# Kernel tuning notes

Hardware: AMD Instinct MI355X
Metric: run time of the kernel (lower is better)

Reference implementation:

```python
import jax, jax.numpy as jnp
import numpy as np

BITS = 4        # int4_fullrange
NPACK = 8       # 32-bit container / 4-bit values
BLOCK = 64      # quantization group size (blocksize)
MASK = (1 << BITS) - 1


def _unpack(packed):
    """Unpack int32 words into NPACK 4-bit unsigned values along the last dim.
    packed: (..., P) int32 -> (..., P*NPACK) int32 in [0, 15]."""
    shifts = jnp.arange(NPACK, dtype=jnp.int32) * BITS  # (8,)
    vals = (packed[..., None] >> shifts) & MASK          # (..., P, 8)
    return vals.reshape(*packed.shape[:-1], packed.shape[-1] * NPACK)


def setup_inputs() -> dict:
    key = jax.random.key(0)
    k1, k2, k3, k4, k5 = jax.random.split(key, 5)
    tokens, in_f, out_f = 4096, 4096, 11008
    groups = in_f // BLOCK                      # 64
    x = jax.random.normal(k1, (tokens, in_f), jnp.float32)
    qweight = jax.random.randint(k2, (out_f, in_f // NPACK), 0, 2147483647, jnp.int32)
    qzeros = jax.random.randint(k3, (out_f, groups // NPACK), 0, 2147483647, jnp.int32)
    scales = jax.random.uniform(k4, (out_f, groups), jnp.float32, 0.001, 0.01)
    bias = jax.random.normal(k5, (out_f,), jnp.float32)
    return {"x": x, "qweight": qweight, "qzeros": qzeros, "scales": scales, "bias": bias}


def reference(x, qweight, qzeros, scales, bias):
    # Recover fp32 weight: w[o, g*BLOCK + b] = scales[o, g] * (w_int - zp[o, g])
    out_f, groups = scales.shape
    w_int = _unpack(qweight).astype(jnp.float32)           # (out, in)
    zp = _unpack(qzeros).astype(jnp.float32)               # (out, groups)
    w = (w_int.reshape(out_f, groups, BLOCK) - zp[:, :, None]) * scales[:, :, None]
    w = w.reshape(out_f, groups * BLOCK)                   # (out, in)
    # F.linear(x, w, bias)
    return x @ w.T + bias
```

## Files before the change

### kernel.cpp

```cpp
#include <hip/hip_runtime.h>
#include <stdint.h>

#define M_TOK 4096
#define K_IN  4096
#define N_OUT 11008
#define GROUPS 64
#define WPR 512

#define BM 256
#define BN 256
#define BK 64
#define TM (M_TOK / BM)
#define TN (N_OUT / BN)
#define NWG (TM * TN)
#define KTILES (K_IN / BK)

typedef __bf16 bf16x8 __attribute__((ext_vector_type(8)));
typedef float  f32x4  __attribute__((ext_vector_type(4)));

__device__ __forceinline__ uint16_t f2bf(float f) {
  uint32_t u = __float_as_uint(f);
  u += 0x7FFFu + ((u >> 16) & 1u);
  return (uint16_t)(u >> 16);
}

#define XBLK ((M_TOK * K_IN) / (256 * 8))
#define WBLK ((N_OUT * WPR) / 256)

__global__ __launch_bounds__(256) void prep(const float* __restrict__ x,
                                            const uint32_t* __restrict__ qw,
                                            const uint32_t* __restrict__ qz,
                                            const float* __restrict__ sc,
                                            uint16_t* __restrict__ xb,
                                            uint16_t* __restrict__ wb) {
  if (blockIdx.x < XBLK) {
    size_t i = ((size_t)blockIdx.x * 256 + threadIdx.x) * 8;
    const float4* p = (const float4*)(x + i);
    float4 a = p[0];
    float4 b = p[1];
    uint4 v;
    v.x = (uint32_t)f2bf(a.x) | ((uint32_t)f2bf(a.y) << 16);
    v.y = (uint32_t)f2bf(a.z) | ((uint32_t)f2bf(a.w) << 16);
    v.z = (uint32_t)f2bf(b.x) | ((uint32_t)f2bf(b.y) << 16);
    v.w = (uint32_t)f2bf(b.z) | ((uint32_t)f2bf(b.w) << 16);
    *(uint4*)(xb + i) = v;
  } else {
    int idx = (blockIdx.x - XBLK) * 256 + threadIdx.x;
    int o = idx >> 9;
    int p = idx & 511;
    int g = p >> 3;
    uint32_t zw = qz[o * (GROUPS / 8) + (g >> 3)];
    float zp = (float)((zw >> ((g & 7) * 4)) & 15u);
    float s = sc[o * GROUPS + g];
    float c = -s * zp;
    uint32_t w = qw[idx];
    uint4 v;
    uint32_t r[4];
#pragma unroll
    for (int j = 0; j < 4; j++) {
      float f0 = (float)((w >> (8 * j)) & 15u);
      float f1 = (float)((w >> (8 * j + 4)) & 15u);
      r[j] = (uint32_t)f2bf(fmaf(f0, s, c)) | ((uint32_t)f2bf(fmaf(f1, s, c)) << 16);
    }
    v.x = r[0]; v.y = r[1]; v.z = r[2]; v.w = r[3];
    *(uint4*)(wb + (size_t)idx * 8) = v;
  }
}

#define SBAR()   __builtin_amdgcn_s_barrier()
#define SCHED0() __builtin_amdgcn_sched_barrier(0)
#define WAITV(n) asm volatile("s_waitcnt vmcnt(" #n ")" ::: "memory")
#define WAITL0() asm volatile("s_waitcnt lgkmcnt(0)" ::: "memory")

#define STAGE_A(buf, half, kt) do {                                            \
  _Pragma("unroll")                                                            \
  for (int c_ = 0; c_ < 2; c_++) {                                             \
    const int r_ = (half) * 128 + c_ * 64 + wave * 8;                          \
    __builtin_amdgcn_global_load_lds(                                          \
        (const __attribute__((address_space(1))) uint32_t*)(                   \
            gA + (size_t)r_ * K_IN + (size_t)(kt) * BK),                       \
        (__attribute__((address_space(3))) uint32_t*)(&As[(buf)][r_][0]),      \
        16, 0, 0);                                                             \
  } } while (0)

#define STAGE_B(buf, half, kt) do {                                            \
  _Pragma("unroll")                                                            \
  for (int c_ = 0; c_ < 2; c_++) {                                             \
    const int r_ = (half) * 128 + c_ * 64 + wave * 8;                          \
    __builtin_amdgcn_global_load_lds(                                          \
        (const __attribute__((address_space(1))) uint32_t*)(                   \
            gB + (size_t)r_ * K_IN + (size_t)(kt) * BK),                       \
        (__attribute__((address_space(3))) uint32_t*)(&Bs[(buf)][r_][0]),      \
        16, 0, 0);                                                             \
  } } while (0)

#define LOAD_A(buf, mh) do {                                                   \
  _Pragma("unroll")                                                            \
  for (int i2_ = 0; i2_ < 4; i2_++) {                                          \
    const int row_ = (mh) * 128 + wm * 64 + i2_ * 16 + col;                    \
    af[i2_][0] = *(const bf16x8*)&As[(buf)][row_][(quad ^ cs) << 3];           \
    af[i2_][1] = *(const bf16x8*)&As[(buf)][row_][((4 + quad) ^ cs) << 3];     \
  } } while (0)

#define LOAD_B(buf, nh) do {                                                   \
  _Pragma("unroll")                                                            \
  for (int j2_ = 0; j2_ < 2; j2_++) {                                          \
    const int row_ = (nh) * 128 + wn * 32 + j2_ * 16 + col;                    \
    bfr[j2_][0] = *(const bf16x8*)&Bs[(buf)][row_][(quad ^ cs) << 3];          \
    bfr[j2_][1] = *(const bf16x8*)&Bs[(buf)][row_][((4 + quad) ^ cs) << 3];    \
  } } while (0)

#define MMA(mh, nh) do {                                                       \
  __builtin_amdgcn_s_setprio(1);                                               \
  _Pragma("unroll")                                                            \
  for (int i2_ = 0; i2_ < 4; i2_++)                                            \
    _Pragma("unroll")                                                          \
    for (int j2_ = 0; j2_ < 2; j2_++) {                                        \
      acc[(mh)*4 + i2_][(nh)*2 + j2_] = __builtin_amdgcn_mfma_f32_16x16x32_bf16( \
          af[i2_][0], bfr[j2_][0], acc[(mh)*4 + i2_][(nh)*2 + j2_], 0, 0, 0);  \
      acc[(mh)*4 + i2_][(nh)*2 + j2_] = __builtin_amdgcn_mfma_f32_16x16x32_bf16( \
          af[i2_][1], bfr[j2_][1], acc[(mh)*4 + i2_][(nh)*2 + j2_], 0, 0, 0);  \
    }                                                                          \
  __builtin_amdgcn_s_setprio(0); } while (0)

__global__ __launch_bounds__(512, 2) void gemm_bf16(const uint16_t* __restrict__ A,
                                                    const uint16_t* __restrict__ B,
                                                    const float* __restrict__ bias,
                                                    float* __restrict__ C) {
  __shared__ __align__(16) uint16_t As[2][BM][BK];
  __shared__ __align__(16) uint16_t Bs[2][BN][BK];

  const int bid = blockIdx.x;
  const int wg  = (bid & 7) * (NWG / 8) + (bid >> 3);
  const int mt  = wg / TN;
  const int nt  = wg % TN;
  const size_t m0 = (size_t)mt * BM;
  const size_t n0 = (size_t)nt * BN;

  const int tid  = threadIdx.x;
  const int wave = tid >> 6;
  const int lane = tid & 63;
  const int wm   = wave >> 2;
  const int wn   = wave & 3;
  const int lrow = lane >> 3;
  const int lcol = lane & 7;
  const int col  = lane & 15;
  const int quad = lane >> 4;
  const int cs   = col & 7;

  const uint16_t* gA = A + (m0 + lrow) * K_IN + (size_t)((lcol ^ lrow) << 3);
  const uint16_t* gB = B + (n0 + lrow) * K_IN + (size_t)((lcol ^ lrow) << 3);

  f32x4 acc[8][4];
#pragma unroll
  for (int i = 0; i < 8; i++)
#pragma unroll
    for (int j = 0; j < 4; j++)
      acc[i][j] = (f32x4){0.f, 0.f, 0.f, 0.f};

  bf16x8 af[4][2];
  bf16x8 bfr[2][2];

  STAGE_A(0, 0, 0); STAGE_B(0, 1, 0); STAGE_A(0, 1, 0); STAGE_B(0, 0, 0);
  STAGE_A(1, 0, 1); STAGE_B(1, 1, 1);
  WAITV(4);
  SBAR(); SCHED0();

  for (int it = 0; it < KTILES / 2 - 1; ++it) {
    const int kt = 2 * it;
    LOAD_A(0, 0); LOAD_B(0, 0);
    STAGE_A(1, 1, kt + 1);
    SBAR(); WAITL0(); SCHED0();
    MMA(0, 0);
    SBAR(); SCHED0();
    LOAD_B(0, 1);
    STAGE_B(1, 0, kt + 1);
    SBAR(); WAITL0(); SCHED0();
    MMA(0, 1);
    SBAR(); SCHED0();
    LOAD_A(0, 1);
    STAGE_A(0, 0, kt + 2);
    SBAR(); WAITL0(); SCHED0();
    MMA(1, 1);
    SBAR(); SCHED0();
    LOAD_B(0, 0);
    STAGE_B(0, 1, kt + 2);
    SBAR(); WAITL0(); SCHED0();
    MMA(1, 0);
    WAITV(4);
    SBAR(); SCHED0();
    LOAD_A(1, 0); LOAD_B(1, 0);
    STAGE_A(0, 1, kt + 2);
    SBAR(); WAITL0(); SCHED0();
    MMA(0, 0);
    SBAR(); SCHED0();
    LOAD_B(1, 1);
    STAGE_B(0, 0, kt + 2);
    SBAR(); WAITL0(); SCHED0();
    MMA(0, 1);
    SBAR(); SCHED0();
    LOAD_A(1, 1);
    STAGE_A(1, 0, kt + 3);
    SBAR(); WAITL0(); SCHED0();
    MMA(1, 1);
    SBAR(); SCHED0();
    LOAD_B(1, 0);
    STAGE_B(1, 1, kt + 3);
    SBAR(); WAITL0(); SCHED0();
    MMA(1, 0);
    WAITV(4);
    SBAR(); SCHED0();
  }

  LOAD_A(0, 0); LOAD_B(0, 0);
  STAGE_A(1, 1, KTILES - 1);
  SBAR(); WAITL0(); SCHED0();
  MMA(0, 0);
  SBAR(); SCHED0();
  LOAD_B(0, 1);
  STAGE_B(1, 0, KTILES - 1);
  SBAR(); WAITL0(); SCHED0();
  MMA(0, 1);
  SBAR(); SCHED0();
  LOAD_A(0, 1);
  SBAR(); WAITL0(); SCHED0();
  MMA(1, 1);
  SBAR(); SCHED0();
  LOAD_B(0, 0);
  SBAR(); WAITL0(); SCHED0();
  MMA(1, 0);
  WAITV(0);
  SBAR(); SCHED0();
  LOAD_A(1, 0); LOAD_B(1, 0);
  SBAR(); WAITL0(); SCHED0();
  MMA(0, 0);
  SBAR(); SCHED0();
  LOAD_B(1, 1);
  SBAR(); WAITL0(); SCHED0();
  MMA(0, 1);
  SBAR(); SCHED0();
  LOAD_A(1, 1);
  SBAR(); WAITL0(); SCHED0();
  MMA(1, 1);
  SBAR(); SCHED0();
  LOAD_B(1, 0);
  SBAR(); WAITL0(); SCHED0();
  MMA(1, 0);

#pragma unroll
  for (int i = 0; i < 8; i++) {
    const int mrow = (int)m0 + (i >> 2) * 128 + wm * 64 + (i & 3) * 16 + quad * 4;
#pragma unroll
    for (int j = 0; j < 4; j++) {
      const int ncol = (int)n0 + (j >> 1) * 128 + wn * 32 + (j & 1) * 16 + col;
      const float bv = bias[ncol];
      float* out = C + (size_t)mrow * N_OUT + ncol;
#pragma unroll
      for (int r = 0; r < 4; r++)
        __builtin_nontemporal_store(acc[i][j][r] + bv, out + (size_t)r * N_OUT);
    }
  }
}

__global__ __launch_bounds__(256) void fallback_fused(const float* __restrict__ x,
                                                      const uint32_t* __restrict__ qw,
                                                      const uint32_t* __restrict__ qz,
                                                      const float* __restrict__ sc,
                                                      const float* __restrict__ bias,
                                                      float* __restrict__ out) {
  __shared__ float xs[K_IN];
  const int t = blockIdx.y;
  const int o = blockIdx.x * 256 + threadIdx.x;
  for (int i = threadIdx.x; i < K_IN; i += 256) xs[i] = x[(size_t)t * K_IN + i];
  __syncthreads();
  float acc = 0.f;
  const uint32_t* qwr = qw + (size_t)o * WPR;
  for (int g = 0; g < GROUPS; g++) {
    uint32_t zw = qz[o * (GROUPS / 8) + (g >> 3)];
    float zp = (float)((zw >> ((g & 7) * 4)) & 15u);
    float s = sc[o * GROUPS + g];
    float gacc = 0.f, gsum = 0.f;
    for (int w = 0; w < 8; w++) {
      uint32_t wv = qwr[g * 8 + w];
#pragma unroll
      for (int j = 0; j < 8; j++) {
        float xv = xs[g * 64 + w * 8 + j];
        gacc = fmaf((float)((wv >> (4 * j)) & 15u), xv, gacc);
        gsum += xv;
      }
    }
    acc += s * (gacc - zp * gsum);
  }
  out[(size_t)t * N_OUT + o] = acc + bias[o];
}

extern "C" void kernel_launch(void* const* d_in, const int* in_sizes, int n_in,
                              void* d_out, int out_size, void* d_ws, size_t ws_size,
                              hipStream_t stream) {
  (void)in_sizes; (void)n_in; (void)out_size;
  const float*    x    = (const float*)d_in[0];
  const uint32_t* qw   = (const uint32_t*)d_in[1];
  const uint32_t* qz   = (const uint32_t*)d_in[2];
  const float*    sc   = (const float*)d_in[3];
  const float*    bias = (const float*)d_in[4];
  float* out = (float*)d_out;

  const size_t xb_bytes = (size_t)M_TOK * K_IN * 2;
  const size_t wb_bytes = (size_t)N_OUT * K_IN * 2;

  if (ws_size >= xb_bytes + wb_bytes) {
    uint16_t* xb = (uint16_t*)d_ws;
    uint16_t* wb = (uint16_t*)((char*)d_ws + xb_bytes);
    prep<<<XBLK + WBLK, 256, 0, stream>>>(x, qw, qz, sc, xb, wb);
    gemm_bf16<<<NWG, 512, 0, stream>>>(xb, wb, bias, out);
  } else {
    fallback_fused<<<dim3(N_OUT / 256, M_TOK), 256, 0, stream>>>(x, qw, qz, sc, bias, out);
  }
}
```

Baseline: 633.7 us.

## Reorder LDS staging to split vmcnt waits and widen dequant per-thread work

The GEMM main loop reorders the global-to-LDS staging of A and B half-tiles and splits the single vmcnt wait into two finer-grained waits (8 and 6 outstanding). This lets compute begin on half-tiles that have already landed while later loads are still in flight. Separately, the weight dequant prep kernel now has each thread process four packed words strided by 128 instead of one, using a quarter as many blocks. The finer waits add synchronisation points, and any mistake in counting outstanding loads would cause data races.

```diff
diff --git a/kernel.cpp b/kernel.cpp
--- a/kernel.cpp
+++ b/kernel.cpp
@@ -25,7 +25,7 @@
 }
 
 #define XBLK ((M_TOK * K_IN) / (256 * 8))
-#define WBLK ((N_OUT * WPR) / 256)
+#define WBLK ((N_OUT * WPR) / (256 * 4))
 
 __global__ __launch_bounds__(256) void prep(const float* __restrict__ x,
                                             const uint32_t* __restrict__ qw,
@@ -45,25 +45,31 @@
     v.w = (uint32_t)f2bf(b.z) | ((uint32_t)f2bf(b.w) << 16);
     *(uint4*)(xb + i) = v;
   } else {
-    int idx = (blockIdx.x - XBLK) * 256 + threadIdx.x;
-    int o = idx >> 9;
-    int p = idx & 511;
-    int g = p >> 3;
-    uint32_t zw = qz[o * (GROUPS / 8) + (g >> 3)];
-    float zp = (float)((zw >> ((g & 7) * 4)) & 15u);
-    float s = sc[o * GROUPS + g];
-    float c = -s * zp;
-    uint32_t w = qw[idx];
-    uint4 v;
-    uint32_t r[4];
+    int t = (blockIdx.x - XBLK) * 256 + threadIdx.x;
+    int o  = t >> 7;
+    int p0 = t & 127;
+    const uint32_t* qwr = qw + (size_t)o * WPR + p0;
+    uint16_t* wbr = wb + ((size_t)o * WPR + p0) * 8;
 #pragma unroll
     for (int j = 0; j < 4; j++) {
-      float f0 = (float)((w >> (8 * j)) & 15u);
-      float f1 = (float)((w >> (8 * j + 4)) & 15u);
-      r[j] = (uint32_t)f2bf(fmaf(f0, s, c)) | ((uint32_t)f2bf(fmaf(f1, s, c)) << 16);
+      int p = p0 + j * 128;
+      int g = p >> 3;
+      uint32_t zw = qz[o * (GROUPS / 8) + (g >> 3)];
+      float zp = (float)((zw >> ((g & 7) * 4)) & 15u);
+      float s = sc[o * GROUPS + g];
+      float c = -s * zp;
+      uint32_t w = qwr[j * 128];
+      uint4 v;
+      uint32_t r[4];
+#pragma unroll
+      for (int q = 0; q < 4; q++) {
+        float f0 = (float)((w >> (8 * q)) & 15u);
+        float f1 = (float)((w >> (8 * q + 4)) & 15u);
+        r[q] = (uint32_t)f2bf(fmaf(f0, s, c)) | ((uint32_t)f2bf(fmaf(f1, s, c)) << 16);
+      }
+      v.x = r[0]; v.y = r[1]; v.z = r[2]; v.w = r[3];
+      *(uint4*)(wbr + (size_t)j * 128 * 8) = v;
     }
-    v.x = r[0]; v.y = r[1]; v.z = r[2]; v.w = r[3];
-    *(uint4*)(wb + (size_t)idx * 8) = v;
   }
 }
 
@@ -161,22 +167,23 @@
   bf16x8 af[4][2];
   bf16x8 bfr[2][2];
 
-  STAGE_A(0, 0, 0); STAGE_B(0, 1, 0); STAGE_A(0, 1, 0); STAGE_B(0, 0, 0);
+  STAGE_A(0, 0, 0); STAGE_B(0, 1, 0); STAGE_B(0, 0, 0); STAGE_A(0, 1, 0);
   STAGE_A(1, 0, 1); STAGE_B(1, 1, 1);
-  WAITV(4);
+  WAITV(6);
   SBAR(); SCHED0();
 
   for (int it = 0; it < KTILES / 2 - 1; ++it) {
     const int kt = 2 * it;
     LOAD_A(0, 0); LOAD_B(0, 0);
+    STAGE_B(1, 0, kt + 1);
+    SBAR(); WAITL0(); SCHED0();
+    MMA(0, 0);
+    SBAR(); SCHED0();
+    LOAD_B(0, 1);
     STAGE_A(1, 1, kt + 1);
     SBAR(); WAITL0(); SCHED0();
-    MMA(0, 0);
-    SBAR(); SCHED0();
-    LOAD_B(0, 1);
-    STAGE_B(1, 0, kt + 1);
-    SBAR(); WAITL0(); SCHED0();
     MMA(0, 1);
+    WAITV(8);
     SBAR(); SCHED0();
     LOAD_A(0, 1);
     STAGE_A(0, 0, kt + 2);
@@ -187,17 +194,18 @@
     STAGE_B(0, 1, kt + 2);
     SBAR(); WAITL0(); SCHED0();
     MMA(1, 0);
-    WAITV(4);
+    WAITV(6);
     SBAR(); SCHED0();
     LOAD_A(1, 0); LOAD_B(1, 0);
+    STAGE_B(0, 0, kt + 2);
+    SBAR(); WAITL0(); SCHED0();
+    MMA(0, 0);
+    SBAR(); SCHED0();
+    LOAD_B(1, 1);
     STAGE_A(0, 1, kt + 2);
     SBAR(); WAITL0(); SCHED0();
-    MMA(0, 0);
-    SBAR(); SCHED0();
-    LOAD_B(1, 1);
-    STAGE_B(0, 0, kt + 2);
-    SBAR(); WAITL0(); SCHED0();
     MMA(0, 1);
+    WAITV(8);
     SBAR(); SCHED0();
     LOAD_A(1, 1);
     STAGE_A(1, 0, kt + 3);
@@ -208,36 +216,38 @@
     STAGE_B(1, 1, kt + 3);
     SBAR(); WAITL0(); SCHED0();
     MMA(1, 0);
-    WAITV(4);
+    WAITV(6);
     SBAR(); SCHED0();
   }
 
   LOAD_A(0, 0); LOAD_B(0, 0);
+  STAGE_B(1, 0, KTILES - 1);
+  SBAR(); WAITL0(); SCHED0();
+  MMA(0, 0);
+  SBAR(); SCHED0();
+  LOAD_B(0, 1);
   STAGE_A(1, 1, KTILES - 1);
   SBAR(); WAITL0(); SCHED0();
+  MMA(0, 1);
+  WAITV(8);
+  SBAR(); SCHED0();
+  LOAD_A(0, 1);
+  SBAR(); WAITL0(); SCHED0();
+  MMA(1, 1);
+  SBAR(); SCHED0();
+  LOAD_B(0, 0);
+  SBAR(); WAITL0(); SCHED0();
+  MMA(1, 0);
+  WAITV(2);
+  SBAR(); SCHED0();
+  LOAD_A(1, 0); LOAD_B(1, 0);
+  SBAR(); WAITL0(); SCHED0();
   MMA(0, 0);
   SBAR(); SCHED0();
-  LOAD_B(0, 1);
-  STAGE_B(1, 0, KTILES - 1);
+  LOAD_B(1, 1);
   SBAR(); WAITL0(); SCHED0();
   MMA(0, 1);
-  SBAR(); SCHED0();
-  LOAD_A(0, 1);
-  SBAR(); WAITL0(); SCHED0();
-  MMA(1, 1);
-  SBAR(); SCHED0();
-  LOAD_B(0, 0);
-  SBAR(); WAITL0(); SCHED0();
-  MMA(1, 0);
   WAITV(0);
-  SBAR(); SCHED0();
-  LOAD_A(1, 0); LOAD_B(1, 0);
-  SBAR(); WAITL0(); SCHED0();
-  MMA(0, 0);
-  SBAR(); SCHED0();
-  LOAD_B(1, 1);
-  SBAR(); WAITL0(); SCHED0();
-  MMA(0, 1);
   SBAR(); SCHED0();
   LOAD_A(1, 1);
   SBAR(); WAITL0(); SCHED0();
```

Result: faster. 579.3 us (-8.6%).
